# Kernel optimization log

Measured on AMD Instinct MI355X. Metric: run time of the kernel, lower is better.

Reference implementation:

```python
import jax, jax.numpy as jnp
import numpy as np
from jax import lax

HIDDEN_CH = 32
KS = 3


def _conv(x, w):
    # x: [B, Cin, H, W], w: [Cout, Cin, k, k] -> [B, Cout, H, W] (SAME padding)
    return lax.conv_general_dilated(
        x, w, window_strides=(1, 1), padding='SAME',
        dimension_numbers=('NCHW', 'OIHW', 'NCHW'))


def _cell(x, h, gw, gb, cw, cb):
    combined = jnp.concatenate([x, h], axis=1)
    gates = jax.nn.sigmoid(_conv(combined, gw) + gb[None, :, None, None])
    r, z = jnp.split(gates, 2, axis=1)
    combined_r = jnp.concatenate([x, r * h], axis=1)
    n = jnp.tanh(_conv(combined_r, cw) + cb[None, :, None, None])
    return (1.0 - z) * h + z * n


def setup_inputs() -> dict:
    key = jax.random.key(0)
    ks = jax.random.split(key, 9)
    B, T, H, W = 8, 16, 128, 128
    hc = HIDDEN_CH
    seq = jax.random.normal(ks[0], (B, T, H, W), dtype=jnp.float32)

    def conv_init(k, cout, cin):
        fan_in = cin * KS * KS
        bound = 1.0 / np.sqrt(fan_in)
        return jax.random.uniform(k, (cout, cin, KS, KS), jnp.float32, -bound, bound)

    def bias_init(k, cout, cin):
        bound = 1.0 / np.sqrt(cin * KS * KS)
        return jax.random.uniform(k, (cout,), jnp.float32, -bound, bound)

    # Layer 0: input_ch=1, layer 1: input_ch=hc
    gw0 = conv_init(ks[1], 2 * hc, 1 + hc)
    gb0 = bias_init(ks[2], 2 * hc, 1 + hc)
    cw0 = conv_init(ks[3], hc, 1 + hc)
    cb0 = bias_init(ks[4], hc, 1 + hc)
    gw1 = conv_init(ks[5], 2 * hc, hc + hc)
    gb1 = bias_init(ks[6], 2 * hc, hc + hc)
    cw1 = conv_init(ks[7], hc, hc + hc)
    cb1 = bias_init(ks[8], hc, hc + hc)
    return {'seq': seq, 'gw0': gw0, 'gb0': gb0, 'cw0': cw0, 'cb0': cb0,
            'gw1': gw1, 'gb1': gb1, 'cw1': cw1, 'cb1': cb1}


def reference(seq, gw0, gb0, cw0, cb0, gw1, gb1, cw1, cb1):
    B, T, H, W = seq.shape
    hc = HIDDEN_CH
    h0 = jnp.zeros((B, hc, H, W), dtype=seq.dtype)
    h1 = jnp.zeros((B, hc, H, W), dtype=seq.dtype)
    # xs: [T, B, 1, H, W]
    xs = jnp.transpose(seq, (1, 0, 2, 3))[:, :, None, :, :]

    def step(carry, x_t):
        h0, h1 = carry
        h0 = _cell(x_t, h0, gw0, gb0, cw0, cb0)
        h1 = _cell(h0, h1, gw1, gb1, cw1, cb1)
        return (h0, h1), None

    (h0, h1), _ = lax.scan(step, (h0, h1), xs)
    return h1
```

## Files before the change

### kernel.cpp

```cpp
#include <hip/hip_runtime.h>


#define HH 128
#define PH 130
#define HW 16384
#define BB 8
#define TT 16

typedef _Float16 f16x8 __attribute__((ext_vector_type(8)));
typedef float f32x4 __attribute__((ext_vector_type(4)));
typedef unsigned int u32x4 __attribute__((ext_vector_type(4)));

__device__ __forceinline__ unsigned short f2h(float x){
    return __builtin_bit_cast(unsigned short, (_Float16)x);
}
__device__ __forceinline__ float h2f(unsigned short u){
    return (float)__builtin_bit_cast(_Float16, u);
}
__device__ __forceinline__ f16x8 ld_frag(const unsigned short* p){
    u32x4 v = *(const u32x4*)p;
    return __builtin_bit_cast(f16x8, v);
}
__device__ __forceinline__ f16x8 lds_frag_w(const unsigned short* base, int spix, int q){
    u32x4 v = *(const u32x4*)(base + spix * 32 + q * 8);
    return __builtin_bit_cast(f16x8, v);
}
__device__ __forceinline__ float sigmoid_f(float a){ return 1.0f / (1.0f + __expf(-a)); }
__device__ __forceinline__ float tanh_f(float a){ float e2 = __expf(2.0f * a); return 1.0f - 2.0f / (e2 + 1.0f); }

struct SmemT {
    unsigned short hs[2][13824];
    unsigned short rh[10880];
    float xt[444];
};

__device__ __forceinline__ void halo_rc10(int s, int& gr, int& gc){
    s = s > 83 ? 83 : s;
    if (s < 34)      { gr = 0;            gc = s;      }
    else if (s < 68) { gr = 9;            gc = s - 34; }
    else if (s < 76) { gr = 1 + (s - 68); gc = 0;      }
    else             { gr = 1 + (s - 76); gc = 33;     }
}

__device__ __forceinline__ f16x8 x_im2col(const float* xt, int gr, int gc, int q){
    f16x8 v;
#pragma unroll
    for (int j = 0; j < 8; ++j) {
        int k = q * 8 + j;
        float f = 0.0f;
        if (k < 9) f = xt[(gr + k / 3) * 37 + gc + k % 3];
        v[j] = (_Float16)f;
    }
    return v;
}

__device__ __forceinline__ void stage_plane12(unsigned short* slot,
    const unsigned short* __restrict__ g, int b, int pr0, int pc0)
{
    const int wv = threadIdx.x >> 6, lane = threadIdx.x & 63;
    for (int k = wv; k < 27; k += 8) {
        int chunk = k * 64 + lane;
        int pix = chunk >> 2, part = chunk & 3;
        int r = pix / 36, c = pix - r * 36;
        int pr = pr0 + r; pr = pr < 0 ? 0 : (pr > 129 ? 129 : pr);
        int pc = pc0 + c; pc = pc < 0 ? 0 : (pc > 129 ? 129 : pc);
        const unsigned short* ga = g + ((long)((b * PH + pr) * PH + pc) * 32 + part * 8);
        __builtin_amdgcn_global_load_lds(
            (const __attribute__((address_space(1))) unsigned int*)ga,
            (__attribute__((address_space(3))) unsigned int*)(slot + k * 512),
            16, 0, 0);
    }
}

__global__ void prep_w(const float* __restrict__ w, unsigned short* __restrict__ wf,
                       int CO, int CIT, int NSTEP, int xmode)
{
    int idx = blockIdx.x * 256 + threadIdx.x;
    int total = NSTEP * CO * 32;
    if (idx >= total) return;
    int kk = idx & 31;
    int t  = idx >> 5;
    int co = t % CO;
    int s  = t / CO;
    float v = 0.0f;
    if (xmode && s == NSTEP - 1) {
        if (kk < 9) v = w[(co * CIT + 0) * 9 + kk];
    } else {
        int tap = s % 9;
        int cin = (s / 9) * 32 + kk + (xmode ? 1 : 0);
        v = w[(co * CIT + cin) * 9 + tap];
    }
    wf[idx] = f2h(v);
}

template<int L, int EMIT>
__device__ __forceinline__ void do_cell(SmemT& sm,
    const unsigned short* __restrict__ Hin,
    unsigned short* __restrict__ Hout,
    const unsigned short* __restrict__ Xin,
    const float* __restrict__ seq, int t,
    const unsigned short* __restrict__ Wg, const float* __restrict__ bg,
    const unsigned short* __restrict__ Wc, const float* __restrict__ bc,
    float* __restrict__ out, int b, int R0, int C0)
{
    constexpr int KG = (L == 0) ? 10 : 18;
    constexpr int KC = (L == 0) ? 10 : 18;

    if (L == 0) {
        stage_plane12(sm.hs[0], Hin, b, R0 - 1, C0 - 1);
        if (threadIdx.x < 444) {
            int p = threadIdx.x;
            int r = p / 37, c = p - r * 37;
            int ir = R0 - 2 + r, ic = C0 - 2 + c;
            float v = 0.0f;
            if (ir >= 0 && ir < HH && ic >= 0 && ic < HH)
                v = seq[((long)b * TT + t) * HW + ir * HH + ic];
            sm.xt[p] = v;
        }
    } else {
        stage_plane12(sm.hs[0], Xin, b, R0 - 1, C0 - 1);
        stage_plane12(sm.hs[1], Hin, b, R0 - 1, C0 - 1);
    }
    __syncthreads();

    const int wv = threadIdx.x >> 6, lane = threadIdx.x & 63;
    const int m16 = lane & 15, q = lane >> 4;
    const unsigned short* hp = (L == 0) ? sm.hs[0] : sm.hs[1];

    const bool HASH = (wv >= 2);
    int hgr = 0, hgc = 0;
    halo_rc10((wv - 2) * 16 + m16, hgr, hgc);

    f32x4 gI[2][4];
    f32x4 gH[2];
#pragma unroll
    for (int ng = 0; ng < 4; ++ng) {
        float bv = bg[ng * 16 + m16];
#pragma unroll
        for (int mg = 0; mg < 2; ++mg) gI[mg][ng] = f32x4{bv, bv, bv, bv};
        if (ng < 2) gH[ng] = f32x4{bv, bv, bv, bv};
    }

    f16x8 Bc[4];
#pragma unroll
    for (int ng = 0; ng < 4; ++ng)
        Bc[ng] = ld_frag(Wg + (ng * 16 + m16) * 32 + q * 8);

#pragma unroll
    for (int s = 0; s < KG; ++s) {
        f16x8 Bn[4];
        if (s + 1 < KG) {
#pragma unroll
            for (int ng = 0; ng < 4; ++ng)
                Bn[ng] = ld_frag(Wg + ((s + 1) * 64 + ng * 16 + m16) * 32 + q * 8);
        }
        f16x8 AI[2], AH;
        if (L == 0 && s == 9) {
#pragma unroll
            for (int mg = 0; mg < 2; ++mg)
                AI[mg] = x_im2col(sm.xt, wv + 1, mg * 16 + 1 + m16, q);
            AH = x_im2col(sm.xt, hgr, hgc, q);
        } else {
            const int tap = (L == 0) ? s : (s % 9);
            const unsigned short* pl = (L == 1 && s >= 9) ? sm.hs[1] : sm.hs[0];
#pragma unroll
            for (int mg = 0; mg < 2; ++mg)
                AI[mg] = lds_frag_w(pl, (wv + 1 + tap / 3) * 36 + mg * 16 + 1 + m16 + tap % 3, q);
            AH = lds_frag_w(pl, (hgr + tap / 3) * 36 + hgc + tap % 3, q);
        }
#pragma unroll
        for (int mg = 0; mg < 2; ++mg)
#pragma unroll
            for (int ng = 0; ng < 4; ++ng)
                gI[mg][ng] = __builtin_amdgcn_mfma_f32_16x16x32_f16(AI[mg], Bc[ng], gI[mg][ng], 0, 0, 0);
        if (HASH) {
#pragma unroll
            for (int ng = 0; ng < 2; ++ng)
                gH[ng] = __builtin_amdgcn_mfma_f32_16x16x32_f16(AH, Bc[ng], gH[ng], 0, 0, 0);
        }
        if (s + 1 < KG) {
#pragma unroll
            for (int ng = 0; ng < 4; ++ng) Bc[ng] = Bn[ng];
        }
    }

    unsigned int zpk[2][4];
#pragma unroll
    for (int mg = 0; mg < 2; ++mg)
#pragma unroll
        for (int rg = 0; rg < 4; ++rg) {
            int gr = wv + 1, gc = mg * 16 + 1 + q * 4 + rg;
            zpk[mg][rg] = (unsigned int)f2h(sigmoid_f(gI[mg][2][rg]))
                        | ((unsigned int)f2h(sigmoid_f(gI[mg][3][rg])) << 16);
#pragma unroll
            for (int ng = 0; ng < 2; ++ng) {
                int n = ng * 16 + m16;
                float rv = sigmoid_f(gI[mg][ng][rg]);
                float hv = h2f(hp[((gr + 1) * 36 + gc + 1) * 32 + n]);
                sm.rh[(gr * 34 + gc) * 32 + n] = f2h(rv * hv);
            }
        }
    if (HASH) {
#pragma unroll
        for (int rg = 0; rg < 4; ++rg) {
            int gr, gc; halo_rc10((wv - 2) * 16 + q * 4 + rg, gr, gc);
#pragma unroll
            for (int ng = 0; ng < 2; ++ng) {
                int n = ng * 16 + m16;
                float rv = sigmoid_f(gH[ng][rg]);
                float hv = h2f(hp[((gr + 1) * 36 + gc + 1) * 32 + n]);
                sm.rh[(gr * 34 + gc) * 32 + n] = f2h(rv * hv);
            }
        }
    }
    __syncthreads();

    f32x4 cacc[2][2];
#pragma unroll
    for (int mg = 0; mg < 2; ++mg)
#pragma unroll
        for (int ng = 0; ng < 2; ++ng) {
            float bv = bc[ng * 16 + m16];
            cacc[mg][ng] = f32x4{bv, bv, bv, bv};
        }
    f16x8 Cc[2];
#pragma unroll
    for (int ng = 0; ng < 2; ++ng)
        Cc[ng] = ld_frag(Wc + (ng * 16 + m16) * 32 + q * 8);
#pragma unroll
    for (int s = 0; s < KC; ++s) {
        f16x8 Cn[2];
        if (s + 1 < KC) {
#pragma unroll
            for (int ng = 0; ng < 2; ++ng)
                Cn[ng] = ld_frag(Wc + ((s + 1) * 32 + ng * 16 + m16) * 32 + q * 8);
        }
        f16x8 A2[2];
        if (L == 0 && s == 9) {
#pragma unroll
            for (int mg = 0; mg < 2; ++mg)
                A2[mg] = x_im2col(sm.xt, wv + 1, mg * 16 + 1 + m16, q);
        } else if (L == 1 && s < 9) {
#pragma unroll
            for (int mg = 0; mg < 2; ++mg)
                A2[mg] = lds_frag_w(sm.hs[0], (wv + 1 + s / 3) * 36 + mg * 16 + m16 + 1 + s % 3, q);
        } else {
            const int tap = (L == 0) ? s : (s - 9);
#pragma unroll
            for (int mg = 0; mg < 2; ++mg)
                A2[mg] = lds_frag_w(sm.rh, (wv + tap / 3) * 34 + mg * 16 + m16 + tap % 3, q);
        }
#pragma unroll
        for (int mg = 0; mg < 2; ++mg)
#pragma unroll
            for (int ng = 0; ng < 2; ++ng)
                cacc[mg][ng] = __builtin_amdgcn_mfma_f32_16x16x32_f16(A2[mg], Cc[ng], cacc[mg][ng], 0, 0, 0);
        if (s + 1 < KC) {
#pragma unroll
            for (int ng = 0; ng < 2; ++ng) Cc[ng] = Cn[ng];
        }
    }

    unsigned short hvout[2][2][4];
#pragma unroll
    for (int mg = 0; mg < 2; ++mg)
#pragma unroll
        for (int ng = 0; ng < 2; ++ng)
#pragma unroll
            for (int rg = 0; rg < 4; ++rg) {
                int lcol = mg * 16 + q * 4 + rg;
                int n = ng * 16 + m16;
                float nv = tanh_f(cacc[mg][ng][rg]);
                float zz = h2f((unsigned short)(zpk[mg][rg] >> (ng * 16)));
                float ho = h2f(hp[((wv + 2) * 36 + lcol + 2) * 32 + n]);
                float hnew = (1.0f - zz) * ho + zz * nv;
                if (!EMIT) {
                    long psp = (long)(b * PH + R0 + wv + 1) * PH + (C0 + lcol + 1);
                    Hout[psp * 32 + n] = f2h(hnew);
                } else {
                    hvout[mg][ng][rg] = f2h(hnew);
                }
            }

    if (EMIT) {
        __syncthreads();
        unsigned short* scr = sm.rh;
#pragma unroll
        for (int mg = 0; mg < 2; ++mg)
#pragma unroll
            for (int ng = 0; ng < 2; ++ng)
#pragma unroll
                for (int rg = 0; rg < 4; ++rg)
                    scr[((wv * 32 + mg * 16 + q * 4 + rg) * 32) + ng * 16 + m16] = hvout[mg][ng][rg];
        __syncthreads();
        const int tid = threadIdx.x;
        const int rowid = tid >> 1, half = tid & 1;
        const int n = rowid >> 3, wr = rowid & 7;
        long obase = ((long)(b * 32 + n) * HH + (R0 + wr)) * HH + C0 + half * 16;
#pragma unroll
        for (int j = 0; j < 16; ++j)
            out[obase + j] = h2f(scr[(wr * 32 + half * 16 + j) * 32 + n]);
    }
}

__global__ __launch_bounds__(512, 4)
void cell_l0(const unsigned short* __restrict__ Hin, unsigned short* __restrict__ Hout,
             const float* __restrict__ seq, int t,
             const unsigned short* __restrict__ Wg, const float* __restrict__ bg,
             const unsigned short* __restrict__ Wc, const float* __restrict__ bc)
{
    __shared__ __align__(16) SmemT sm;
    const int wg = blockIdx.x;
    const int b = wg >> 6, tr = (wg >> 2) & 15, tc = wg & 3;
    do_cell<0, 0>(sm, Hin, Hout, (const unsigned short*)0, seq, t,
                  Wg, bg, Wc, bc, (float*)0, b, tr * 8, tc * 32);
}

__global__ __launch_bounds__(512, 4)
void step_pair(const unsigned short* __restrict__ h1r, unsigned short* __restrict__ h1w,
               const unsigned short* __restrict__ h0r, unsigned short* __restrict__ h0w,
               const float* __restrict__ seq, int tnext,
               const unsigned short* __restrict__ WG0, const float* __restrict__ gb0,
               const unsigned short* __restrict__ WC0, const float* __restrict__ cb0,
               const unsigned short* __restrict__ WG1, const float* __restrict__ gb1,
               const unsigned short* __restrict__ WC1, const float* __restrict__ cb1)
{
    __shared__ __align__(16) SmemT sm;
    const int wg = blockIdx.x;
    const int b = wg >> 6, tr = (wg >> 2) & 15, tc = wg & 3;
    if (blockIdx.z == 0)
        do_cell<1, 0>(sm, h1r, h1w, h0r, seq, 0,
                      WG1, gb1, WC1, cb1, (float*)0, b, tr * 8, tc * 32);
    else
        do_cell<0, 0>(sm, h0r, h0w, (const unsigned short*)0, seq, tnext,
                      WG0, gb0, WC0, cb0, (float*)0, b, tr * 8, tc * 32);
}

__global__ __launch_bounds__(512, 4)
void cell_l1_emit(const unsigned short* __restrict__ Hin,
                  const unsigned short* __restrict__ Xin,
                  const unsigned short* __restrict__ Wg, const float* __restrict__ bg,
                  const unsigned short* __restrict__ Wc, const float* __restrict__ bc,
                  float* __restrict__ out)
{
    __shared__ __align__(16) SmemT sm;
    const int wg = blockIdx.x;
    const int b = wg >> 6, tr = (wg >> 2) & 15, tc = wg & 3;
    do_cell<1, 1>(sm, Hin, (unsigned short*)0, Xin, (const float*)0, 0,
                  Wg, bg, Wc, bc, out, b, tr * 8, tc * 32);
}

extern "C" void kernel_launch(void* const* d_in, const int* in_sizes, int n_in,
                              void* d_out, int out_size, void* d_ws, size_t ws_size,
                              hipStream_t stream)
{
    const float* seq = (const float*)d_in[0];
    const float* gw0 = (const float*)d_in[1];
    const float* gb0 = (const float*)d_in[2];
    const float* cw0 = (const float*)d_in[3];
    const float* cb0 = (const float*)d_in[4];
    const float* gw1 = (const float*)d_in[5];
    const float* gb1 = (const float*)d_in[6];
    const float* cw1 = (const float*)d_in[7];
    const float* cb1 = (const float*)d_in[8];
    float* out = (float*)d_out;

    const size_t NSP = (size_t)BB * PH * PH * 32;

    char* p = (char*)d_ws;
    unsigned short* S0A = (unsigned short*)p; p += NSP * 2;
    unsigned short* S0B = (unsigned short*)p; p += NSP * 2;
    unsigned short* S1A = (unsigned short*)p; p += NSP * 2;
    unsigned short* S1B = (unsigned short*)p; p += NSP * 2;
    unsigned short* WG0 = (unsigned short*)p; p += 20480 * 2;
    unsigned short* WC0 = (unsigned short*)p; p += 10240 * 2;
    unsigned short* WG1 = (unsigned short*)p; p += 36864 * 2;
    unsigned short* WC1 = (unsigned short*)p; p += 18432 * 2;

    hipMemsetAsync(S0A, 0, 4 * NSP * 2, stream);

    prep_w<<<(10 * 64 * 32 + 255) / 256, 256, 0, stream>>>(gw0, WG0, 64, 33, 10, 1);
    prep_w<<<(10 * 32 * 32 + 255) / 256, 256, 0, stream>>>(cw0, WC0, 32, 33, 10, 1);
    prep_w<<<(18 * 64 * 32 + 255) / 256, 256, 0, stream>>>(gw1, WG1, 64, 64, 18, 0);
    prep_w<<<(18 * 32 * 32 + 255) / 256, 256, 0, stream>>>(cw1, WC1, 32, 64, 18, 0);

    dim3 grid1(512, 1, 1), grid2(512, 1, 2), block(512);

    cell_l0<<<grid1, block, 0, stream>>>(S0A, S0B, seq, 0, WG0, gb0, WC0, cb0);

    unsigned short *h0r = S0B, *h0w = S0A, *h1r = S1A, *h1w = S1B;
    for (int t = 0; t < TT - 1; ++t) {
        step_pair<<<grid2, block, 0, stream>>>(h1r, h1w, h0r, h0w, seq, t + 1,
                                               WG0, gb0, WC0, cb0,
                                               WG1, gb1, WC1, cb1);
        unsigned short* tmp;
        tmp = h0r; h0r = h0w; h0w = tmp;
        tmp = h1r; h1r = h1w; h1w = tmp;
    }
    cell_l1_emit<<<grid1, block, 0, stream>>>(h1r, h0r, WG1, gb1, WC1, cb1, out);
}
```

Baseline: 966.8 us.

## Fuse layer-1 and layer-0 cells into one block sharing the staged h0 tile

Replaces the two-slice step_pair grid, where each block computed either the layer-1 or the layer-0 cell, with a fused_pair kernel. Each block stages the h0 tile, the h1 tile and the input tile once, then computes the layer-1 cell followed by the layer-0 cell on the same shared-memory data. This avoids loading the h0 halo tile twice per step. In exchange the grid halves to 512 blocks, each doing twice the serial work, which may leave CU slots idle and reduce latency hiding. The layer-0 pass also relies on the layer-1 pass leaving the staged h0 tile in shared memory intact.

Measured after the change: 1.005 ms. 3.9% more time.

```diff
diff --git a/kernel.cpp b/kernel.cpp
--- a/kernel.cpp
+++ b/kernel.cpp
@@ -69,6 +69,20 @@
             (const __attribute__((address_space(1))) unsigned int*)ga,
             (__attribute__((address_space(3))) unsigned int*)(slot + k * 512),
             16, 0, 0);
+    }
+}
+
+__device__ __forceinline__ void stage_x12(float* xt, const float* __restrict__ seq,
+                                          int b, int t, int R0, int C0)
+{
+    if (threadIdx.x < 444) {
+        int p = threadIdx.x;
+        int r = p / 37, c = p - r * 37;
+        int ir = R0 - 2 + r, ic = C0 - 2 + c;
+        float v = 0.0f;
+        if (ir >= 0 && ir < HH && ic >= 0 && ic < HH)
+            v = seq[((long)b * TT + t) * HW + ir * HH + ic];
+        xt[p] = v;
     }
 }
 
@@ -94,34 +108,14 @@
 }
 
 template<int L, int EMIT>
-__device__ __forceinline__ void do_cell(SmemT& sm,
-    const unsigned short* __restrict__ Hin,
+__device__ __forceinline__ void cell_compute(SmemT& sm,
     unsigned short* __restrict__ Hout,
-    const unsigned short* __restrict__ Xin,
-    const float* __restrict__ seq, int t,
     const unsigned short* __restrict__ Wg, const float* __restrict__ bg,
     const unsigned short* __restrict__ Wc, const float* __restrict__ bc,
     float* __restrict__ out, int b, int R0, int C0)
 {
     constexpr int KG = (L == 0) ? 10 : 18;
     constexpr int KC = (L == 0) ? 10 : 18;
-
-    if (L == 0) {
-        stage_plane12(sm.hs[0], Hin, b, R0 - 1, C0 - 1);
-        if (threadIdx.x < 444) {
-            int p = threadIdx.x;
-            int r = p / 37, c = p - r * 37;
-            int ir = R0 - 2 + r, ic = C0 - 2 + c;
-            float v = 0.0f;
-            if (ir >= 0 && ir < HH && ic >= 0 && ic < HH)
-                v = seq[((long)b * TT + t) * HW + ir * HH + ic];
-            sm.xt[p] = v;
-        }
-    } else {
-        stage_plane12(sm.hs[0], Xin, b, R0 - 1, C0 - 1);
-        stage_plane12(sm.hs[1], Hin, b, R0 - 1, C0 - 1);
-    }
-    __syncthreads();
 
     const int wv = threadIdx.x >> 6, lane = threadIdx.x & 63;
     const int m16 = lane & 15, q = lane >> 4;
@@ -312,28 +306,33 @@
     __shared__ __align__(16) SmemT sm;
     const int wg = blockIdx.x;
     const int b = wg >> 6, tr = (wg >> 2) & 15, tc = wg & 3;
-    do_cell<0, 0>(sm, Hin, Hout, (const unsigned short*)0, seq, t,
-                  Wg, bg, Wc, bc, (float*)0, b, tr * 8, tc * 32);
+    const int R0 = tr * 8, C0 = tc * 32;
+    stage_x12(sm.xt, seq, b, t, R0, C0);
+    stage_plane12(sm.hs[0], Hin, b, R0 - 1, C0 - 1);
+    __syncthreads();
+    cell_compute<0, 0>(sm, Hout, Wg, bg, Wc, bc, (float*)0, b, R0, C0);
 }
 
 __global__ __launch_bounds__(512, 4)
-void step_pair(const unsigned short* __restrict__ h1r, unsigned short* __restrict__ h1w,
-               const unsigned short* __restrict__ h0r, unsigned short* __restrict__ h0w,
-               const float* __restrict__ seq, int tnext,
-               const unsigned short* __restrict__ WG0, const float* __restrict__ gb0,
-               const unsigned short* __restrict__ WC0, const float* __restrict__ cb0,
-               const unsigned short* __restrict__ WG1, const float* __restrict__ gb1,
-               const unsigned short* __restrict__ WC1, const float* __restrict__ cb1)
+void fused_pair(const unsigned short* __restrict__ h1r, unsigned short* __restrict__ h1w,
+                const unsigned short* __restrict__ h0r, unsigned short* __restrict__ h0w,
+                const float* __restrict__ seq, int tnext,
+                const unsigned short* __restrict__ WG0, const float* __restrict__ gb0,
+                const unsigned short* __restrict__ WC0, const float* __restrict__ cb0,
+                const unsigned short* __restrict__ WG1, const float* __restrict__ gb1,
+                const unsigned short* __restrict__ WC1, const float* __restrict__ cb1)
 {
     __shared__ __align__(16) SmemT sm;
     const int wg = blockIdx.x;
     const int b = wg >> 6, tr = (wg >> 2) & 15, tc = wg & 3;
-    if (blockIdx.z == 0)
-        do_cell<1, 0>(sm, h1r, h1w, h0r, seq, 0,
-                      WG1, gb1, WC1, cb1, (float*)0, b, tr * 8, tc * 32);
-    else
-        do_cell<0, 0>(sm, h0r, h0w, (const unsigned short*)0, seq, tnext,
-                      WG0, gb0, WC0, cb0, (float*)0, b, tr * 8, tc * 32);
+    const int R0 = tr * 8, C0 = tc * 32;
+    stage_x12(sm.xt, seq, b, tnext, R0, C0);
+    stage_plane12(sm.hs[0], h0r, b, R0 - 1, C0 - 1);
+    stage_plane12(sm.hs[1], h1r, b, R0 - 1, C0 - 1);
+    __syncthreads();
+    cell_compute<1, 0>(sm, h1w, WG1, gb1, WC1, cb1, (float*)0, b, R0, C0);
+    __syncthreads();
+    cell_compute<0, 0>(sm, h0w, WG0, gb0, WC0, cb0, (float*)0, b, R0, C0);
 }
 
 __global__ __launch_bounds__(512, 4)
@@ -346,8 +345,11 @@
     __shared__ __align__(16) SmemT sm;
     const int wg = blockIdx.x;
     const int b = wg >> 6, tr = (wg >> 2) & 15, tc = wg & 3;
-    do_cell<1, 1>(sm, Hin, (unsigned short*)0, Xin, (const float*)0, 0,
-                  Wg, bg, Wc, bc, out, b, tr * 8, tc * 32);
+    const int R0 = tr * 8, C0 = tc * 32;
+    stage_plane12(sm.hs[0], Xin, b, R0 - 1, C0 - 1);
+    stage_plane12(sm.hs[1], Hin, b, R0 - 1, C0 - 1);
+    __syncthreads();
+    cell_compute<1, 1>(sm, (unsigned short*)0, Wg, bg, Wc, bc, out, b, R0, C0);
 }
 
 extern "C" void kernel_launch(void* const* d_in, const int* in_sizes, int n_in,
@@ -384,18 +386,18 @@
     prep_w<<<(18 * 64 * 32 + 255) / 256, 256, 0, stream>>>(gw1, WG1, 64, 64, 18, 0);
     prep_w<<<(18 * 32 * 32 + 255) / 256, 256, 0, stream>>>(cw1, WC1, 32, 64, 18, 0);
 
-    dim3 grid1(512, 1, 1), grid2(512, 1, 2), block(512);
-
-    cell_l0<<<grid1, block, 0, stream>>>(S0A, S0B, seq, 0, WG0, gb0, WC0, cb0);
+    dim3 grid(512, 1, 1), block(512);
+
+    cell_l0<<<grid, block, 0, stream>>>(S0A, S0B, seq, 0, WG0, gb0, WC0, cb0);
 
     unsigned short *h0r = S0B, *h0w = S0A, *h1r = S1A, *h1w = S1B;
     for (int t = 0; t < TT - 1; ++t) {
-        step_pair<<<grid2, block, 0, stream>>>(h1r, h1w, h0r, h0w, seq, t + 1,
+        fused_pair<<<grid, block, 0, stream>>>(h1r, h1w, h0r, h0w, seq, t + 1,
                                                WG0, gb0, WC0, cb0,
                                                WG1, gb1, WC1, cb1);
         unsigned short* tmp;
         tmp = h0r; h0r = h0w; h0w = tmp;
         tmp = h1r; h1r = h1w; h1w = tmp;
     }
-    cell_l1_emit<<<grid1, block, 0, stream>>>(h1r, h0r, WG1, gb1, WC1, cb1, out);
-}
+    cell_l1_emit<<<grid, block, 0, stream>>>(h1r, h0r, WG1, gb1, WC1, cb1, out);
+}
```
